# Kernel tuning notes

Hardware: AMD Instinct MI355X
Metric: run time of the kernel (lower is better)

## Reference

```python
import jax, jax.numpy as jnp
import numpy as np

VOCAB, DIM, HID, OUT = 400000, 300, 32, 2
BATCH, SEQ = 16384, 50

def setup_inputs() -> dict:
    key = jax.random.key(0)
    k_tok, k_emb, k_vw, k_vb, k_ww, k_wb = jax.random.split(key, 6)
    tokens = jax.random.randint(k_tok, (BATCH, SEQ), 0, VOCAB, dtype=jnp.int32)
    emb = jax.random.normal(k_emb, (VOCAB, DIM), dtype=jnp.float32) * 0.02
    emb = emb.at[0].set(0.0)  # padding_idx=0 row conventionally zero
    V_w = jax.random.normal(k_vw, (HID, DIM), dtype=jnp.float32) * (1.0 / np.sqrt(DIM))
    V_b = jnp.zeros((HID,), dtype=jnp.float32)
    W_w = jax.random.normal(k_ww, (OUT, HID), dtype=jnp.float32) * (1.0 / np.sqrt(HID))
    W_b = jnp.zeros((OUT,), dtype=jnp.float32)
    return {"tokens": tokens, "emb": emb, "V_w": V_w, "V_b": V_b, "W_w": W_w, "W_b": W_b}

def reference(tokens, emb, V_w, V_b, W_w, W_b):
    # gather [B,S,D] then mean-pool over words -> [B,D] (DAN average)
    pooled = jnp.mean(emb[tokens], axis=1)
    h = jax.nn.relu(pooled @ V_w.T + V_b)          # [B,HID]
    logits = h @ W_w.T + W_b                        # [B,OUT]
    # original module uses LogSoftmax(dim=0): normalize over the batch axis
    return jax.nn.log_softmax(logits, axis=0)
```

## Files before the change

kernel.cpp:

```cpp
#include <hip/hip_runtime.h>

#define VOCAB 400000
#define DIM   300
#define HID   32
#define NOUT  2
#define BATCH 16384
#define SEQ   50

__global__ __launch_bounds__(256, 8) void dan_main(
    const int*   __restrict__ tokens,
    const float* __restrict__ emb,
    const float* __restrict__ Vw,
    const float* __restrict__ Vb,
    const float* __restrict__ Ww,
    const float* __restrict__ Wb,
    float*       __restrict__ logits)
{
    const int wave = threadIdx.x >> 6;
    const int lane = threadIdx.x & 63;
    const int row  = blockIdx.x * 4 + wave;

    const int* toks = tokens + row * SEQ;
    const bool has1 = (lane < (DIM / 4 - 64));

    float4 acc0 = make_float4(0.f, 0.f, 0.f, 0.f);
    float4 acc1 = make_float4(0.f, 0.f, 0.f, 0.f);

    #pragma unroll 5
    for (int s = 0; s < SEQ; ++s) {
        const int t = toks[s];
        const float4* e = (const float4*)(emb + (size_t)t * DIM);
        float4 v0 = e[lane];
        acc0.x += v0.x; acc0.y += v0.y; acc0.z += v0.z; acc0.w += v0.w;
        if (has1) {
            float4 v1 = e[64 + lane];
            acc1.x += v1.x; acc1.y += v1.y; acc1.z += v1.z; acc1.w += v1.w;
        }
    }
    const float inv = 1.0f / (float)SEQ;
    acc0.x *= inv; acc0.y *= inv; acc0.z *= inv; acc0.w *= inv;

    __shared__ float pool[4][304];
    *(float4*)&pool[wave][4 * lane] = acc0;
    if (has1) {
        acc1.x *= inv; acc1.y *= inv; acc1.z *= inv; acc1.w *= inv;
        *(float4*)&pool[wave][256 + 4 * lane] = acc1;
    }
    __syncthreads();

    const int k    = lane & 31;
    const int half = lane >> 5;
    const int base = half ? 152 : 0;
    const float* __restrict__ vrow = Vw + k * DIM + base;
    const float* pw = &pool[wave][base];

    float p = 0.f;
    #pragma unroll
    for (int i = 0; i < 37; ++i) {
        float4 a = *(const float4*)(pw + 4 * i);
        float4 w = *(const float4*)(vrow + 4 * i);
        p += a.x * w.x + a.y * w.y + a.z * w.z + a.w * w.w;
    }
    if (!half) {
        float4 a = *(const float4*)(pw + 148);
        float4 w = *(const float4*)(vrow + 148);
        p += a.x * w.x + a.y * w.y + a.z * w.z + a.w * w.w;
    }
    p += __shfl_xor(p, 32, 64);

    float hv = fmaxf(p + Vb[k], 0.f);
    float g0 = hv * Ww[k];
    float g1 = hv * Ww[HID + k];
    #pragma unroll
    for (int m = 1; m < 32; m <<= 1) {
        g0 += __shfl_xor(g0, m, 64);
        g1 += __shfl_xor(g1, m, 64);
    }
    if (lane == 0) {
        logits[row * 2 + 0] = g0 + Wb[0];
        logits[row * 2 + 1] = g1 + Wb[1];
    }
}

__global__ __launch_bounds__(1024) void dan_reduce_final(
    const float* __restrict__ logits, float* __restrict__ out)
{
    __shared__ float r0[1024];
    __shared__ float r1[1024];
    const int tid = threadIdx.x;

    float m0 = -INFINITY, m1 = -INFINITY;
    for (int b = tid; b < BATCH; b += 1024) {
        m0 = fmaxf(m0, logits[b * 2 + 0]);
        m1 = fmaxf(m1, logits[b * 2 + 1]);
    }
    r0[tid] = m0; r1[tid] = m1;
    __syncthreads();
    for (int s = 512; s > 0; s >>= 1) {
        if (tid < s) {
            r0[tid] = fmaxf(r0[tid], r0[tid + s]);
            r1[tid] = fmaxf(r1[tid], r1[tid + s]);
        }
        __syncthreads();
    }
    m0 = r0[0]; m1 = r1[0];
    __syncthreads();

    float s0 = 0.f, s1 = 0.f;
    for (int b = tid; b < BATCH; b += 1024) {
        s0 += __expf(logits[b * 2 + 0] - m0);
        s1 += __expf(logits[b * 2 + 1] - m1);
    }
    r0[tid] = s0; r1[tid] = s1;
    __syncthreads();
    for (int s = 512; s > 0; s >>= 1) {
        if (tid < s) {
            r0[tid] += r0[tid + s];
            r1[tid] += r1[tid + s];
        }
        __syncthreads();
    }
    const float c0 = m0 + __logf(r0[0]);
    const float c1 = m1 + __logf(r1[0]);
    for (int i = tid; i < BATCH * NOUT; i += 1024) {
        out[i] = logits[i] - ((i & 1) ? c1 : c0);
    }
}

extern "C" void kernel_launch(void* const* d_in, const int* in_sizes, int n_in,
                              void* d_out, int out_size, void* d_ws, size_t ws_size,
                              hipStream_t stream) {
    const int*   tokens = (const int*)  d_in[0];
    const float* emb    = (const float*)d_in[1];
    const float* Vw     = (const float*)d_in[2];
    const float* Vb     = (const float*)d_in[3];
    const float* Ww     = (const float*)d_in[4];
    const float* Wb     = (const float*)d_in[5];
    float* out    = (float*)d_out;
    float* logits = (float*)d_ws;

    dan_main        <<<BATCH / 4, 256, 0, stream>>>(tokens, emb, Vw, Vb, Ww, Wb, logits);
    dan_reduce_final<<<1, 1024, 0, stream>>>(logits, out);
}
```

Baseline: 742.8 us.

## Prefetch embedding rows into an LDS ring buffer with async global-to-LDS loads

```diff
diff --git a/kernel.cpp b/kernel.cpp
--- a/kernel.cpp
+++ b/kernel.cpp
@@ -7,7 +7,16 @@
 #define BATCH 16384
 #define SEQ   50
 
-__global__ __launch_bounds__(256, 8) void dan_main(
+#define NSLOT     8
+#define LOOKAHEAD 6
+
+__device__ __forceinline__ void gload_lds16(const float* gsrc, float* ldst) {
+    __builtin_amdgcn_global_load_lds(
+        (const __attribute__((address_space(1))) void*)gsrc,
+        (__attribute__((address_space(3))) void*)ldst, 16, 0, 0);
+}
+
+__global__ __launch_bounds__(256, 4) void dan_main(
     const int*   __restrict__ tokens,
     const float* __restrict__ emb,
     const float* __restrict__ Vw,
@@ -23,28 +32,59 @@
     const int* toks = tokens + row * SEQ;
     const bool has1 = (lane < (DIM / 4 - 64));
 
+    __shared__ float gbuf[4][NSLOT][304];
+
+    #pragma unroll
+    for (int s = 0; s < LOOKAHEAD; ++s) {
+        const int t = toks[s];
+        const float* src = emb + (size_t)t * DIM;
+        float* dst = &gbuf[wave][s][0];
+        gload_lds16(src + 4 * lane, dst);
+        if (has1) gload_lds16(src + 4 * (64 + lane), dst + 256);
+    }
+
     float4 acc0 = make_float4(0.f, 0.f, 0.f, 0.f);
     float4 acc1 = make_float4(0.f, 0.f, 0.f, 0.f);
 
-    #pragma unroll 5
-    for (int s = 0; s < SEQ; ++s) {
-        const int t = toks[s];
-        const float4* e = (const float4*)(emb + (size_t)t * DIM);
-        float4 v0 = e[lane];
+    #pragma unroll 2
+    for (int s = 0; s < SEQ - LOOKAHEAD; ++s) {
+        asm volatile("s_waitcnt vmcnt(10)" ::: "memory");
+        __builtin_amdgcn_sched_barrier(0);
+        const float4* sf = (const float4*)&gbuf[wave][s & (NSLOT - 1)][0];
+        float4 v0 = sf[lane];
         acc0.x += v0.x; acc0.y += v0.y; acc0.z += v0.z; acc0.w += v0.w;
         if (has1) {
-            float4 v1 = e[64 + lane];
+            float4 v1 = sf[64 + lane];
+            acc1.x += v1.x; acc1.y += v1.y; acc1.z += v1.z; acc1.w += v1.w;
+        }
+        const int t = toks[s + LOOKAHEAD];
+        const float* src = emb + (size_t)t * DIM;
+        float* dst = &gbuf[wave][(s + LOOKAHEAD) & (NSLOT - 1)][0];
+        gload_lds16(src + 4 * lane, dst);
+        if (has1) gload_lds16(src + 4 * (64 + lane), dst + 256);
+    }
+
+    asm volatile("s_waitcnt vmcnt(0)" ::: "memory");
+    __builtin_amdgcn_sched_barrier(0);
+    #pragma unroll
+    for (int s = SEQ - LOOKAHEAD; s < SEQ; ++s) {
+        const float4* sf = (const float4*)&gbuf[wave][s & (NSLOT - 1)][0];
+        float4 v0 = sf[lane];
+        acc0.x += v0.x; acc0.y += v0.y; acc0.z += v0.z; acc0.w += v0.w;
+        if (has1) {
+            float4 v1 = sf[64 + lane];
             acc1.x += v1.x; acc1.y += v1.y; acc1.z += v1.z; acc1.w += v1.w;
         }
     }
+
     const float inv = 1.0f / (float)SEQ;
     acc0.x *= inv; acc0.y *= inv; acc0.z *= inv; acc0.w *= inv;
 
-    __shared__ float pool[4][304];
-    *(float4*)&pool[wave][4 * lane] = acc0;
+    float* pool = &gbuf[wave][0][0];
+    *(float4*)&pool[4 * lane] = acc0;
     if (has1) {
         acc1.x *= inv; acc1.y *= inv; acc1.z *= inv; acc1.w *= inv;
-        *(float4*)&pool[wave][256 + 4 * lane] = acc1;
+        *(float4*)&pool[256 + 4 * lane] = acc1;
     }
     __syncthreads();
 
@@ -52,7 +92,7 @@
     const int half = lane >> 5;
     const int base = half ? 152 : 0;
     const float* __restrict__ vrow = Vw + k * DIM + base;
-    const float* pw = &pool[wave][base];
+    const float* pw = pool + base;
 
     float p = 0.f;
     #pragma unroll
```

After: 789.7 us. 1.06x slower.
